# Kernel optimization log

Measured on AMD Instinct MI355X. Metric: run time of the kernel, lower is better.

The kernel has to match this reference:

```python
import jax, jax.numpy as jnp
import numpy as np

B, S, D, H, DH, FF = 2, 2048, 2048, 16, 128, 8192
MAXPOS, EPS, NEG = 2048, 1e-5, -1e9


def _ln(x, g, b):
    m = jnp.mean(x, axis=-1, keepdims=True)
    v = jnp.mean(jnp.square(x - m), axis=-1, keepdims=True)
    return (x - m) * jax.lax.rsqrt(v + EPS) * g + b


def _rope_tables():
    # GPT-J sinusoidal table over rotary_dim = DH
    inv_freq = 1.0 / (10000.0 ** (np.arange(0, DH, 2, dtype=np.float32) / DH))
    ang = np.arange(MAXPOS, dtype=np.float32)[:, None] * inv_freq[None, :]  # [P, DH/2]
    return jnp.asarray(np.sin(ang)), jnp.asarray(np.cos(ang))


def _rotate_every_two(t):
    # t: [B,S,H,DH] -> interleaved (-x1, x0, -x3, x2, ...)
    r = jnp.stack((-t[..., 1::2], t[..., ::2]), axis=-1)
    return r.reshape(t.shape)


def _apply_rope(t, sin, cos):
    # sin/cos: [B,S,DH/2] -> repeat_interleave to [B,S,1,DH]
    sin = jnp.repeat(sin, 2, axis=-1)[:, :, None, :]
    cos = jnp.repeat(cos, 2, axis=-1)[:, :, None, :]
    return t * cos + _rotate_every_two(t) * sin


def setup_inputs() -> dict:
    key = jax.random.key(0)
    ks = jax.random.split(key, 8)
    std = 0.02
    w = lambda k, shape: (jax.random.normal(k, shape, jnp.float32) * std)
    return {
        "hidden_states": jax.random.normal(ks[0], (B, S, D), jnp.float32),
        "position_ids": jnp.tile(jnp.arange(S, dtype=jnp.int32), (B, 1)),
        "wq": w(ks[1], (D, D)),
        "wk": w(ks[2], (D, D)),
        "wv": w(ks[3], (D, D)),
        "wo": w(ks[4], (D, D)),
        "ln1_g": jnp.ones((D,), jnp.float32),
        "ln1_b": jnp.zeros((D,), jnp.float32),
        "ln2_g": jnp.ones((D,), jnp.float32),
        "ln2_b": jnp.zeros((D,), jnp.float32),
        "fc_in_w": w(ks[5], (D, FF)),
        "fc_in_b": jnp.zeros((FF,), jnp.float32),
        "fc_out_w": w(ks[6], (FF, D)),
        "fc_out_b": jnp.zeros((D,), jnp.float32),
    }


def reference(hidden_states, position_ids, wq, wk, wv, wo, ln1_g, ln1_b,
              ln2_g, ln2_b, fc_in_w, fc_in_b, fc_out_w, fc_out_b):
    sin_t, cos_t = _rope_tables()
    h = _ln(hidden_states, ln1_g, ln1_b)
    q = (h @ wq).reshape(B, S, H, DH)
    k = (h @ wk).reshape(B, S, H, DH)
    v = (h @ wv).reshape(B, S, H, DH)
    sin = sin_t[position_ids]  # [B,S,DH/2]
    cos = cos_t[position_ids]
    q = _apply_rope(q, sin, cos)
    k = _apply_rope(k, sin, cos)
    # faithful to source: no 1/sqrt(head_dim) scaling
    scores = jnp.einsum("bqhd,bkhd->bhqk", q, k)
    causal = jnp.tril(jnp.ones((S, S), bool))
    scores = jnp.where(causal[None, None], scores, NEG)
    attn_weights = jax.nn.softmax(scores, axis=-1)
    attn = jnp.einsum("bhqk,bkhd->bqhd", attn_weights, v).reshape(B, S, D)
    attn = attn @ wo
    h2 = _ln(hidden_states + attn, ln2_g, ln2_b)
    ffn = jax.nn.gelu(h2 @ fc_in_w + fc_in_b, approximate=False) @ fc_out_w + fc_out_b
    return h2 + ffn, attn_weights
```

## Files before the change

### kernel.cpp

```cpp
#include <hip/hip_runtime.h>
#include <hip/hip_fp16.h>

#define B_ 2
#define S_ 2048
#define D_ 2048
#define H_ 16
#define DH_ 128
#define FF_ 8192

typedef _Float16 f16x8 __attribute__((ext_vector_type(8)));
typedef float f32x4 __attribute__((ext_vector_type(4)));

#define GLD16(gsrc, ldst) __builtin_amdgcn_global_load_lds( \
    (__attribute__((address_space(1))) void*)(uintptr_t)(gsrc), \
    (__attribute__((address_space(3))) void*)(ldst), 16, 0, 0)

__global__ void build_rope_tab(float* __restrict__ tab) {
  const int pos = blockIdx.x;
  const int i = threadIdx.x;
  float ex = (float)(2 * i) / 128.0f;
  float invf = (float)(1.0 / pow(10000.0, (double)ex));
  float ang = (float)pos * invf;
  tab[(size_t)pos * 128 + 2 * i]     = (float)sin((double)ang);
  tab[(size_t)pos * 128 + 2 * i + 1] = (float)cos((double)ang);
}

__global__ void tcast(const float* __restrict__ in, _Float16* __restrict__ out,
                      int R, int C) {
  __shared__ float tile[32][33];
  const int c0 = blockIdx.x * 32, r0 = blockIdx.y * 32;
  const int tx = threadIdx.x, ty = threadIdx.y;
#pragma unroll
  for (int i = 0; i < 32; i += 8)
    tile[ty + i][tx] = in[(size_t)(r0 + ty + i) * C + c0 + tx];
  __syncthreads();
#pragma unroll
  for (int i = 0; i < 32; i += 8)
    out[(size_t)(c0 + ty + i) * R + r0 + tx] = (_Float16)tile[tx][ty + i];
}

__global__ __launch_bounds__(256) void ln_fused(
    const float* __restrict__ x, const float* __restrict__ add,
    const float* __restrict__ g, const float* __restrict__ bv,
    _Float16* __restrict__ outh, float* __restrict__ outf) {
  const int row = blockIdx.x, tid = threadIdx.x;
  const size_t base = (size_t)row * D_;
  const float4* xp = (const float4*)(x + base) + tid * 2;
  float4 a0 = xp[0], a1 = xp[1];
  if (add) {
    const float4* ap = (const float4*)(add + base) + tid * 2;
    float4 b0 = ap[0], b1 = ap[1];
    a0.x += b0.x; a0.y += b0.y; a0.z += b0.z; a0.w += b0.w;
    a1.x += b1.x; a1.y += b1.y; a1.z += b1.z; a1.w += b1.w;
  }
  float v[8] = {a0.x, a0.y, a0.z, a0.w, a1.x, a1.y, a1.z, a1.w};
  float s1 = 0.f, s2 = 0.f;
#pragma unroll
  for (int j = 0; j < 8; ++j) { s1 += v[j]; s2 += v[j] * v[j]; }
#pragma unroll
  for (int off = 32; off; off >>= 1) {
    s1 += __shfl_xor(s1, off);
    s2 += __shfl_xor(s2, off);
  }
  __shared__ float red[8];
  __shared__ float mv[2];
  if ((tid & 63) == 0) { red[tid >> 6] = s1; red[4 + (tid >> 6)] = s2; }
  __syncthreads();
  if (tid == 0) {
    float t1 = red[0] + red[1] + red[2] + red[3];
    float t2 = red[4] + red[5] + red[6] + red[7];
    float mean = t1 * (1.0f / D_);
    float var = t2 * (1.0f / D_) - mean * mean;
    mv[0] = mean; mv[1] = rsqrtf(var + 1e-5f);
  }
  __syncthreads();
  const float mean = mv[0], rstd = mv[1];
  const int c0 = tid * 8;
#pragma unroll
  for (int j = 0; j < 8; ++j) {
    float nv = (v[j] - mean) * rstd * g[c0 + j] + bv[c0 + j];
    outh[base + c0 + j] = (_Float16)nv;
    if (outf) outf[base + c0 + j] = nv;
  }
}

template <int MODE>
__global__ __launch_bounds__(256) void gemm_bt(
    const _Float16* __restrict__ A, const _Float16* __restrict__ Bt,
    float* __restrict__ outF, _Float16* __restrict__ outH,
    const float* __restrict__ bias, const float* __restrict__ res,
    int M, int N, int K) {
  __shared__ _Float16 lsA[128 * 32];
  __shared__ _Float16 lsB[128 * 32];
  const int tid = threadIdx.x;
  const int w = tid >> 6, l = tid & 63;
  const int l4 = l >> 4, l15 = l & 15;
  const int m0 = blockIdx.y * 128, n0 = blockIdx.x * 128;
  const int wm = (w >> 1) * 64, wn = (w & 1) * 64;
  const int srow = l >> 2, schunk = (l & 3) * 8;
  f32x4 acc[4][4] = {};
  for (int k0 = 0; k0 < K; k0 += 32) {
#pragma unroll
    for (int i = 0; i < 2; ++i) {
      const int ai = w * 2 + i;
      const _Float16* ga = A + (size_t)(m0 + ai * 16 + srow) * K + k0 + schunk;
      GLD16(ga, lsA + ai * 512);
      const _Float16* gb = Bt + (size_t)(n0 + ai * 16 + srow) * K + k0 + schunk;
      GLD16(gb, lsB + ai * 512);
    }
    __syncthreads();
    f16x8 af[4], bf[4];
#pragma unroll
    for (int mi = 0; mi < 4; ++mi)
      af[mi] = *(const f16x8*)(lsA + (wm + mi * 16 + l15) * 32 + l4 * 8);
#pragma unroll
    for (int ni = 0; ni < 4; ++ni)
      bf[ni] = *(const f16x8*)(lsB + (wn + ni * 16 + l15) * 32 + l4 * 8);
#pragma unroll
    for (int mi = 0; mi < 4; ++mi)
#pragma unroll
      for (int ni = 0; ni < 4; ++ni)
        acc[mi][ni] = __builtin_amdgcn_mfma_f32_16x16x32_f16(
            af[mi], bf[ni], acc[mi][ni], 0, 0, 0);
    __syncthreads();
  }
#pragma unroll
  for (int mi = 0; mi < 4; ++mi) {
#pragma unroll
    for (int r = 0; r < 4; ++r) {
      const int row = m0 + wm + mi * 16 + l4 * 4 + r;
#pragma unroll
      for (int ni = 0; ni < 4; ++ni) {
        const int col = n0 + wn + ni * 16 + l15;
        float v = acc[mi][ni][r];
        if (MODE == 0) {
          outH[(size_t)row * N + col] = (_Float16)v;
        } else if (MODE == 1) {
          outF[(size_t)row * N + col] = v;
        } else if (MODE == 2) {
          v += bias[col];
          v = 0.5f * v * (1.0f + erff(v * 0.70710678118654752f));
          outH[(size_t)row * N + col] = (_Float16)v;
        } else {
          v += bias[col] + res[(size_t)row * N + col];
          outF[(size_t)row * N + col] = v;
        }
      }
    }
  }
}

__global__ __launch_bounds__(256) void rope_qk(
    const _Float16* __restrict__ qkv, const int* __restrict__ pos_ids,
    const float* __restrict__ tab, _Float16* __restrict__ qr,
    _Float16* __restrict__ kr) {
  const int tid = threadIdx.x, w = tid >> 6, l = tid & 63;
  const int idx = blockIdx.x * 4 + w;
  const int b = idx >> 11, s = idx & 2047;
  const int pos = pos_ids[idx];
  const int h = l >> 2, qtr = l & 3;
  const float* tp = tab + (size_t)pos * 128 + qtr * 32;
  float sn[16], cs[16];
#pragma unroll
  for (int j = 0; j < 16; ++j) { sn[j] = tp[2 * j]; cs[j] = tp[2 * j + 1]; }
#pragma unroll
  for (int sec = 0; sec < 2; ++sec) {
    const _Float16* src = qkv + (size_t)idx * 6144 + sec * 2048 + h * 128 + qtr * 32;
    int4 dv[4];
    const int4* sp = (const int4*)src;
#pragma unroll
    for (int c = 0; c < 4; ++c) dv[c] = sp[c];
    const _Float16* e = (const _Float16*)dv;
    int4 ov[4];
    _Float16* o = (_Float16*)ov;
#pragma unroll
    for (int j = 0; j < 16; ++j) {
      float x0 = (float)e[2 * j], x1 = (float)e[2 * j + 1];
      o[2 * j]     = (_Float16)(x0 * cs[j] - x1 * sn[j]);
      o[2 * j + 1] = (_Float16)(x1 * cs[j] + x0 * sn[j]);
    }
    _Float16* dst = (sec ? kr : qr) + ((size_t)(b * H_ + h) * S_ + s) * DH_ + qtr * 32;
    int4* dp = (int4*)dst;
#pragma unroll
    for (int c = 0; c < 4; ++c) dp[c] = ov[c];
  }
}

__global__ void vtrans(const _Float16* __restrict__ qkv, _Float16* __restrict__ vt) {
  __shared__ _Float16 tile[32][33];
  const int bh = blockIdx.z;
  const int b = bh >> 4, h = bh & 15;
  const int s0 = blockIdx.x * 32, d0 = blockIdx.y * 32;
  const int tx = threadIdx.x, ty = threadIdx.y;
  const _Float16* src = qkv + (size_t)(b * S_) * 6144 + 4096 + h * 128;
#pragma unroll
  for (int i = 0; i < 32; i += 8)
    tile[ty + i][tx] = src[(size_t)(s0 + ty + i) * 6144 + d0 + tx];
  __syncthreads();
  _Float16* dst = vt + (size_t)bh * DH_ * S_;
#pragma unroll
  for (int i = 0; i < 32; i += 8)
    dst[(size_t)(d0 + ty + i) * S_ + s0 + tx] = tile[tx][ty + i];
}

__global__ __launch_bounds__(256) void attn_flash(
    const _Float16* __restrict__ qr, const _Float16* __restrict__ kr,
    const _Float16* __restrict__ vt, _Float16* __restrict__ attnO,
    float* __restrict__ mOut, float* __restrict__ lOut) {
  __shared__ _Float16 kt_lds[64 * 136];
  __shared__ _Float16 vt_lds[128 * 72];
  __shared__ _Float16 p_lds[4 * 16 * 72];
  const int tid = threadIdx.x, w = tid >> 6, l = tid & 63;
  const int l4 = l >> 4, l15 = l & 15;
  const int qt = blockIdx.x, h = blockIdx.y, b = blockIdx.z;
  const int bh = b * H_ + h;
  const int q0 = qt * 64;
  const int qrowA = q0 + w * 16 + l15;
  f16x8 aq[4];
  const _Float16* qbase = qr + ((size_t)bh * S_ + qrowA) * DH_;
#pragma unroll
  for (int ks = 0; ks < 4; ++ks)
    aq[ks] = *(const f16x8*)(qbase + ks * 32 + l4 * 8);
  float m_r[4], l_r[4];
  f32x4 accO[8] = {};
#pragma unroll
  for (int r = 0; r < 4; ++r) { m_r[r] = -1e30f; l_r[r] = 0.f; }
  const int krow = tid >> 2, kc4 = tid & 3;
  const int vdh = tid >> 1, vc = tid & 1;
  _Float16* pw = p_lds + w * 16 * 72;
  for (int kt = 0; kt <= qt; ++kt) {
    const int kbase = kt * 64;
    {
      const _Float16* src = kr + ((size_t)bh * S_ + kbase + krow) * DH_ + kc4 * 32;
      _Float16* dst = kt_lds + krow * 136 + kc4 * 32;
#pragma unroll
      for (int jj = 0; jj < 4; ++jj)
        *(int4*)(dst + jj * 8) = *(const int4*)(src + jj * 8);
      const _Float16* vsrc = vt + ((size_t)bh * DH_ + vdh) * S_ + kbase + vc * 32;
      _Float16* vdst = vt_lds + vdh * 72 + vc * 32;
#pragma unroll
      for (int jj = 0; jj < 4; ++jj)
        *(int4*)(vdst + jj * 8) = *(const int4*)(vsrc + jj * 8);
    }
    __syncthreads();
    f32x4 sc[4] = {};
#pragma unroll
    for (int ni = 0; ni < 4; ++ni)
#pragma unroll
      for (int ks = 0; ks < 4; ++ks) {
        f16x8 bk = *(const f16x8*)(kt_lds + (ni * 16 + l15) * 136 + ks * 32 + l4 * 8);
        sc[ni] = __builtin_amdgcn_mfma_f32_16x16x32_f16(aq[ks], bk, sc[ni], 0, 0, 0);
      }
    if (kt == qt) {
#pragma unroll
      for (int ni = 0; ni < 4; ++ni)
#pragma unroll
        for (int r = 0; r < 4; ++r) {
          const int col = kbase + ni * 16 + l15;
          const int rowq = q0 + w * 16 + l4 * 4 + r;
          if (col > rowq) sc[ni][r] = -1e30f;
        }
    }
    float scale_r[4];
#pragma unroll
    for (int r = 0; r < 4; ++r) {
      float tmax = fmaxf(fmaxf(sc[0][r], sc[1][r]), fmaxf(sc[2][r], sc[3][r]));
#pragma unroll
      for (int off = 1; off < 16; off <<= 1)
        tmax = fmaxf(tmax, __shfl_xor(tmax, off));
      const float mnew = fmaxf(m_r[r], tmax);
      const float scl = __expf(m_r[r] - mnew);
      float ps = 0.f;
#pragma unroll
      for (int ni = 0; ni < 4; ++ni) {
        float pv = __expf(sc[ni][r] - mnew);
        sc[ni][r] = pv;
        ps += pv;
      }
#pragma unroll
      for (int off = 1; off < 16; off <<= 1) ps += __shfl_xor(ps, off);
      l_r[r] = l_r[r] * scl + ps;
      m_r[r] = mnew;
      scale_r[r] = scl;
    }
#pragma unroll
    for (int oi = 0; oi < 8; ++oi)
#pragma unroll
      for (int r = 0; r < 4; ++r) accO[oi][r] *= scale_r[r];
#pragma unroll
    for (int ni = 0; ni < 4; ++ni)
#pragma unroll
      for (int r = 0; r < 4; ++r)
        pw[(l4 * 4 + r) * 72 + ni * 16 + l15] = (_Float16)sc[ni][r];
#pragma unroll
    for (int ks2 = 0; ks2 < 2; ++ks2) {
      f16x8 pa = *(const f16x8*)(pw + l15 * 72 + ks2 * 32 + l4 * 8);
#pragma unroll
      for (int oi = 0; oi < 8; ++oi) {
        f16x8 bv = *(const f16x8*)(vt_lds + (oi * 16 + l15) * 72 + ks2 * 32 + l4 * 8);
        accO[oi] = __builtin_amdgcn_mfma_f32_16x16x32_f16(pa, bv, accO[oi], 0, 0, 0);
      }
    }
    __syncthreads();
  }
#pragma unroll
  for (int r = 0; r < 4; ++r) {
    const float inv = 1.0f / l_r[r];
    const int rowq = q0 + w * 16 + l4 * 4 + r;
#pragma unroll
    for (int oi = 0; oi < 8; ++oi) {
      attnO[((size_t)(b * S_ + rowq) * H_ + h) * DH_ + oi * 16 + l15] =
          (_Float16)(accO[oi][r] * inv);
    }
    if (l15 == 0) {
      mOut[(size_t)bh * S_ + rowq] = m_r[r];
      lOut[(size_t)bh * S_ + rowq] = l_r[r];
    }
  }
}

__global__ __launch_bounds__(256) void attn_pwrite(
    const _Float16* __restrict__ qr, const _Float16* __restrict__ kr,
    const float* __restrict__ mIn, const float* __restrict__ lIn,
    float* __restrict__ outP) {
  __shared__ _Float16 kt_lds[64 * 136];
  const int tid = threadIdx.x, w = tid >> 6, l = tid & 63;
  const int l4 = l >> 4, l15 = l & 15;
  const int kt = blockIdx.x, qt = blockIdx.y, bh = blockIdx.z;
  const int q0 = qt * 64, kbase = kt * 64;
  float* tileout = outP + ((size_t)bh * S_ + q0) * S_ + kbase;
  if (kt > qt) {
    const int r = tid >> 2, cc = (tid & 3) * 16;
    float4 z = {0.f, 0.f, 0.f, 0.f};
    float4* dst = (float4*)(tileout + (size_t)r * S_ + cc);
#pragma unroll
    for (int i = 0; i < 4; ++i) dst[i] = z;
    return;
  }
  {
    const int krow = tid >> 2, kc4 = tid & 3;
    const _Float16* src = kr + ((size_t)bh * S_ + kbase + krow) * DH_ + kc4 * 32;
    _Float16* dst = kt_lds + krow * 136 + kc4 * 32;
#pragma unroll
    for (int jj = 0; jj < 4; ++jj)
      *(int4*)(dst + jj * 8) = *(const int4*)(src + jj * 8);
  }
  const int qrowA = q0 + w * 16 + l15;
  f16x8 aq[4];
  const _Float16* qbase = qr + ((size_t)bh * S_ + qrowA) * DH_;
#pragma unroll
  for (int ks = 0; ks < 4; ++ks)
    aq[ks] = *(const f16x8*)(qbase + ks * 32 + l4 * 8);
  __syncthreads();
  f32x4 sc[4] = {};
#pragma unroll
  for (int ni = 0; ni < 4; ++ni)
#pragma unroll
    for (int ks = 0; ks < 4; ++ks) {
      f16x8 bk = *(const f16x8*)(kt_lds + (ni * 16 + l15) * 136 + ks * 32 + l4 * 8);
      sc[ni] = __builtin_amdgcn_mfma_f32_16x16x32_f16(aq[ks], bk, sc[ni], 0, 0, 0);
    }
  const bool diag = (kt == qt);
#pragma unroll
  for (int r = 0; r < 4; ++r) {
    const int rowq = q0 + w * 16 + l4 * 4 + r;
    const float mv = mIn[(size_t)bh * S_ + rowq];
    const float linv = 1.0f / lIn[(size_t)bh * S_ + rowq];
#pragma unroll
    for (int ni = 0; ni < 4; ++ni) {
      const int col = kbase + ni * 16 + l15;
      float pv = __expf(sc[ni][r] - mv) * linv;
      if (diag && col > rowq) pv = 0.f;
      tileout[(size_t)(w * 16 + l4 * 4 + r) * S_ + ni * 16 + l15] = pv;
    }
  }
}

extern "C" void kernel_launch(void* const* d_in, const int* in_sizes, int n_in,
                              void* d_out, int out_size, void* d_ws, size_t ws_size,
                              hipStream_t stream) {
  (void)in_sizes; (void)n_in; (void)out_size; (void)ws_size;
  const float* hidden   = (const float*)d_in[0];
  const int*   pos_ids  = (const int*)d_in[1];
  const float* wq       = (const float*)d_in[2];
  const float* wk       = (const float*)d_in[3];
  const float* wv       = (const float*)d_in[4];
  const float* wo       = (const float*)d_in[5];
  const float* ln1_g    = (const float*)d_in[6];
  const float* ln1_b    = (const float*)d_in[7];
  const float* ln2_g    = (const float*)d_in[8];
  const float* ln2_b    = (const float*)d_in[9];
  const float* fc_in_w  = (const float*)d_in[10];
  const float* fc_in_b  = (const float*)d_in[11];
  const float* fc_out_w = (const float*)d_in[12];
  const float* fc_out_b = (const float*)d_in[13];

  float* out1 = (float*)d_out;
  float* outP = out1 + (size_t)B_ * S_ * D_;

  char* ws = (char*)d_ws;
  size_t off = 0;
  auto alloc = [&](size_t bytes) {
    char* p = ws + off;
    off += (bytes + 255) & ~(size_t)255;
    return p;
  };
  _Float16* h1h     = (_Float16*)alloc((size_t)4096 * 2048 * 2);
  _Float16* qkvT    = (_Float16*)alloc((size_t)6144 * 2048 * 2);
  _Float16* woT     = (_Float16*)alloc((size_t)2048 * 2048 * 2);
  _Float16* fc_inT  = (_Float16*)alloc((size_t)8192 * 2048 * 2);
  _Float16* fc_outT = (_Float16*)alloc((size_t)2048 * 8192 * 2);
  _Float16* qkv     = (_Float16*)alloc((size_t)4096 * 6144 * 2);
  _Float16* qrB     = (_Float16*)alloc((size_t)32 * 2048 * 128 * 2);
  _Float16* krB     = (_Float16*)alloc((size_t)32 * 2048 * 128 * 2);
  _Float16* vtB     = (_Float16*)alloc((size_t)32 * 128 * 2048 * 2);
  _Float16* attnO   = (_Float16*)alloc((size_t)4096 * 2048 * 2);
  float* mbuf = (float*)alloc((size_t)32 * 2048 * 4);
  float* lbuf = (float*)alloc((size_t)32 * 2048 * 4);
  float* rtab = (float*)alloc((size_t)2048 * 128 * 4);
  float*     attn_out = (float*)h1h;
  _Float16*  ffn1     = qkv;
  float*     h2f      = (float*)krB;
  _Float16*  h2h      = attnO;

  const dim3 tb(32, 8);
  build_rope_tab<<<2048, 64, 0, stream>>>(rtab);
  tcast<<<dim3(64, 64), tb, 0, stream>>>(wq, qkvT, 2048, 2048);
  tcast<<<dim3(64, 64), tb, 0, stream>>>(wk, qkvT + (size_t)2048 * 2048, 2048, 2048);
  tcast<<<dim3(64, 64), tb, 0, stream>>>(wv, qkvT + (size_t)4096 * 2048, 2048, 2048);
  tcast<<<dim3(64, 64), tb, 0, stream>>>(wo, woT, 2048, 2048);
  tcast<<<dim3(256, 64), tb, 0, stream>>>(fc_in_w, fc_inT, 2048, 8192);
  tcast<<<dim3(64, 256), tb, 0, stream>>>(fc_out_w, fc_outT, 8192, 2048);
  ln_fused<<<4096, 256, 0, stream>>>(hidden, nullptr, ln1_g, ln1_b, h1h, nullptr);
  gemm_bt<0><<<dim3(48, 32), 256, 0, stream>>>(h1h, qkvT, nullptr, qkv,
                                               nullptr, nullptr, 4096, 6144, 2048);
  rope_qk<<<1024, 256, 0, stream>>>(qkv, pos_ids, rtab, qrB, krB);
  vtrans<<<dim3(64, 4, 32), tb, 0, stream>>>(qkv, vtB);
  attn_flash<<<dim3(32, 16, 2), 256, 0, stream>>>(qrB, krB, vtB, attnO, mbuf, lbuf);
  attn_pwrite<<<dim3(32, 32, 32), 256, 0, stream>>>(qrB, krB, mbuf, lbuf, outP);
  gemm_bt<1><<<dim3(16, 32), 256, 0, stream>>>(attnO, woT, attn_out, nullptr,
                                               nullptr, nullptr, 4096, 2048, 2048);
  ln_fused<<<4096, 256, 0, stream>>>(hidden, attn_out, ln2_g, ln2_b, h2h, h2f);
  gemm_bt<2><<<dim3(64, 32), 256, 0, stream>>>(h2h, fc_inT, nullptr, ffn1,
                                               fc_in_b, nullptr, 4096, 8192, 2048);
  gemm_bt<3><<<dim3(16, 32), 256, 0, stream>>>(ffn1, fc_outT, out1, nullptr,
                                               fc_out_b, h2f, 4096, 2048, 8192);
}
```

Baseline: 1.785 ms.

## Swizzle block order, XOR-swizzle LDS, prefetch K/V, lazy softmax rescale in attention

The GEMM and flash-attention kernels remap block IDs so consecutive workgroups spread across tiles, likely to improve L2 or XCD locality. The K/V LDS tiles drop row padding and use an XOR swizzle to avoid bank conflicts. The flash kernel now prefetches the next K/V tile into registers while computing the current one. Online softmax only rescales when the running max grows by more than 8, and skips the accumulator rescale when no lane in the wave needs it. These steps add register pressure and rely on the lazy-max threshold staying numerically safe in fp16 P.

```diff
diff --git a/kernel.cpp b/kernel.cpp
--- a/kernel.cpp
+++ b/kernel.cpp
@@ -95,7 +95,11 @@
   const int tid = threadIdx.x;
   const int w = tid >> 6, l = tid & 63;
   const int l4 = l >> 4, l15 = l & 15;
-  const int m0 = blockIdx.y * 128, n0 = blockIdx.x * 128;
+  const int nbx = gridDim.x;
+  const int nwg = nbx * gridDim.y;
+  const int orig = blockIdx.y * nbx + blockIdx.x;
+  const int swz = (orig & 7) * (nwg >> 3) + (orig >> 3);
+  const int m0 = (swz / nbx) * 128, n0 = (swz % nbx) * 128;
   const int wm = (w >> 1) * 64, wn = (w & 1) * 64;
   const int srow = l >> 2, schunk = (l & 3) * 8;
   f32x4 acc[4][4] = {};
@@ -207,14 +211,17 @@
     const _Float16* __restrict__ qr, const _Float16* __restrict__ kr,
     const _Float16* __restrict__ vt, _Float16* __restrict__ attnO,
     float* __restrict__ mOut, float* __restrict__ lOut) {
-  __shared__ _Float16 kt_lds[64 * 136];
-  __shared__ _Float16 vt_lds[128 * 72];
+  __shared__ _Float16 kt_lds[64 * 128];
+  __shared__ _Float16 vt_lds[128 * 64];
   __shared__ _Float16 p_lds[4 * 16 * 72];
   const int tid = threadIdx.x, w = tid >> 6, l = tid & 63;
   const int l4 = l >> 4, l15 = l & 15;
-  const int qt = blockIdx.x, h = blockIdx.y, b = blockIdx.z;
+  const int orig = (blockIdx.z * 16 + blockIdx.y) * 32 + blockIdx.x;
+  const int swzid = (orig & 7) * 128 + (orig >> 3);
+  const int qt = swzid & 31, h = (swzid >> 5) & 15, b = swzid >> 9;
   const int bh = b * H_ + h;
   const int q0 = qt * 64;
+  const int swzk = (l15 & 7) << 4;
   const int qrowA = q0 + w * 16 + l15;
   f16x8 aq[4];
   const _Float16* qbase = qr + ((size_t)bh * S_ + qrowA) * DH_;
@@ -225,30 +232,42 @@
   f32x4 accO[8] = {};
 #pragma unroll
   for (int r = 0; r < 4; ++r) { m_r[r] = -1e30f; l_r[r] = 0.f; }
-  const int krow = tid >> 2, kc4 = tid & 3;
-  const int vdh = tid >> 1, vc = tid & 1;
+  const int krow_s = tid >> 2, kcol_s = (tid & 3) * 32;
+  const int vrow_s = tid >> 1, vcol_s = (tid & 1) * 32;
   _Float16* pw = p_lds + w * 16 * 72;
+  {
+    const _Float16* ksrc = kr + ((size_t)bh * S_ + krow_s) * DH_ + kcol_s;
+    const _Float16* vsrc = vt + ((size_t)bh * DH_ + vrow_s) * S_ + vcol_s;
+#pragma unroll
+    for (int j = 0; j < 4; ++j) {
+      int4 t0 = *(const int4*)(ksrc + j * 8);
+      int4 t1 = *(const int4*)(vsrc + j * 8);
+      *(int4*)((char*)kt_lds + (krow_s * 256 + ((kcol_s * 2 + j * 16) ^ ((krow_s & 7) << 4)))) = t0;
+      *(int4*)((char*)vt_lds + (vrow_s * 128 + ((vcol_s * 2 + j * 16) ^ ((vrow_s & 7) << 4)))) = t1;
+    }
+  }
+  __syncthreads();
   for (int kt = 0; kt <= qt; ++kt) {
     const int kbase = kt * 64;
-    {
-      const _Float16* src = kr + ((size_t)bh * S_ + kbase + krow) * DH_ + kc4 * 32;
-      _Float16* dst = kt_lds + krow * 136 + kc4 * 32;
-#pragma unroll
-      for (int jj = 0; jj < 4; ++jj)
-        *(int4*)(dst + jj * 8) = *(const int4*)(src + jj * 8);
-      const _Float16* vsrc = vt + ((size_t)bh * DH_ + vdh) * S_ + kbase + vc * 32;
-      _Float16* vdst = vt_lds + vdh * 72 + vc * 32;
-#pragma unroll
-      for (int jj = 0; jj < 4; ++jj)
-        *(int4*)(vdst + jj * 8) = *(const int4*)(vsrc + jj * 8);
-    }
-    __syncthreads();
+    const bool pre = (kt < qt);
+    int4 kreg[4], vreg[4];
+    if (pre) {
+      const int kb2 = kbase + 64;
+      const _Float16* ksrc = kr + ((size_t)bh * S_ + kb2 + krow_s) * DH_ + kcol_s;
+      const _Float16* vsrc = vt + ((size_t)bh * DH_ + vrow_s) * S_ + kb2 + vcol_s;
+#pragma unroll
+      for (int j = 0; j < 4; ++j) {
+        kreg[j] = *(const int4*)(ksrc + j * 8);
+        vreg[j] = *(const int4*)(vsrc + j * 8);
+      }
+    }
     f32x4 sc[4] = {};
 #pragma unroll
     for (int ni = 0; ni < 4; ++ni)
 #pragma unroll
       for (int ks = 0; ks < 4; ++ks) {
-        f16x8 bk = *(const f16x8*)(kt_lds + (ni * 16 + l15) * 136 + ks * 32 + l4 * 8);
+        f16x8 bk = *(const f16x8*)((const char*)kt_lds +
+                     ((ni * 16 + l15) * 256 + ((ks * 64 + l4 * 16) ^ swzk)));
         sc[ni] = __builtin_amdgcn_mfma_f32_16x16x32_f16(aq[ks], bk, sc[ni], 0, 0, 0);
       }
     if (kt == qt) {
@@ -262,31 +281,37 @@
         }
     }
     float scale_r[4];
+    bool need = false;
 #pragma unroll
     for (int r = 0; r < 4; ++r) {
       float tmax = fmaxf(fmaxf(sc[0][r], sc[1][r]), fmaxf(sc[2][r], sc[3][r]));
 #pragma unroll
       for (int off = 1; off < 16; off <<= 1)
         tmax = fmaxf(tmax, __shfl_xor(tmax, off));
-      const float mnew = fmaxf(m_r[r], tmax);
-      const float scl = __expf(m_r[r] - mnew);
+      float scl;
+      if (tmax > m_r[r] + 8.0f) {
+        scl = __expf(m_r[r] - tmax); m_r[r] = tmax; need = true;
+      } else {
+        scl = 1.0f;
+      }
       float ps = 0.f;
 #pragma unroll
       for (int ni = 0; ni < 4; ++ni) {
-        float pv = __expf(sc[ni][r] - mnew);
+        float pv = __expf(sc[ni][r] - m_r[r]);
         sc[ni][r] = pv;
         ps += pv;
       }
 #pragma unroll
       for (int off = 1; off < 16; off <<= 1) ps += __shfl_xor(ps, off);
       l_r[r] = l_r[r] * scl + ps;
-      m_r[r] = mnew;
       scale_r[r] = scl;
     }
-#pragma unroll
-    for (int oi = 0; oi < 8; ++oi)
-#pragma unroll
-      for (int r = 0; r < 4; ++r) accO[oi][r] *= scale_r[r];
+    if (__any((int)need)) {
+#pragma unroll
+      for (int oi = 0; oi < 8; ++oi)
+#pragma unroll
+        for (int r = 0; r < 4; ++r) accO[oi][r] *= scale_r[r];
+    }
 #pragma unroll
     for (int ni = 0; ni < 4; ++ni)
 #pragma unroll
@@ -297,11 +322,20 @@
       f16x8 pa = *(const f16x8*)(pw + l15 * 72 + ks2 * 32 + l4 * 8);
 #pragma unroll
       for (int oi = 0; oi < 8; ++oi) {
-        f16x8 bv = *(const f16x8*)(vt_lds + (oi * 16 + l15) * 72 + ks2 * 32 + l4 * 8);
+        f16x8 bv = *(const f16x8*)((const char*)vt_lds +
+                     ((oi * 16 + l15) * 128 + ((ks2 * 64 + l4 * 16) ^ swzk)));
         accO[oi] = __builtin_amdgcn_mfma_f32_16x16x32_f16(pa, bv, accO[oi], 0, 0, 0);
       }
     }
     __syncthreads();
+    if (pre) {
+#pragma unroll
+      for (int j = 0; j < 4; ++j) {
+        *(int4*)((char*)kt_lds + (krow_s * 256 + ((kcol_s * 2 + j * 16) ^ ((krow_s & 7) << 4)))) = kreg[j];
+        *(int4*)((char*)vt_lds + (vrow_s * 128 + ((vcol_s * 2 + j * 16) ^ ((vrow_s & 7) << 4)))) = vreg[j];
+      }
+      __syncthreads();
+    }
   }
 #pragma unroll
   for (int r = 0; r < 4; ++r) {
@@ -323,11 +357,12 @@
     const _Float16* __restrict__ qr, const _Float16* __restrict__ kr,
     const float* __restrict__ mIn, const float* __restrict__ lIn,
     float* __restrict__ outP) {
-  __shared__ _Float16 kt_lds[64 * 136];
+  __shared__ _Float16 kt_lds[64 * 128];
   const int tid = threadIdx.x, w = tid >> 6, l = tid & 63;
   const int l4 = l >> 4, l15 = l & 15;
   const int kt = blockIdx.x, qt = blockIdx.y, bh = blockIdx.z;
   const int q0 = qt * 64, kbase = kt * 64;
+  const int swzk = (l15 & 7) << 4;
   float* tileout = outP + ((size_t)bh * S_ + q0) * S_ + kbase;
   if (kt > qt) {
     const int r = tid >> 2, cc = (tid & 3) * 16;
@@ -338,12 +373,13 @@
     return;
   }
   {
-    const int krow = tid >> 2, kc4 = tid & 3;
-    const _Float16* src = kr + ((size_t)bh * S_ + kbase + krow) * DH_ + kc4 * 32;
-    _Float16* dst = kt_lds + krow * 136 + kc4 * 32;
-#pragma unroll
-    for (int jj = 0; jj < 4; ++jj)
-      *(int4*)(dst + jj * 8) = *(const int4*)(src + jj * 8);
+    const int krow = tid >> 2, kc = (tid & 3) * 32;
+    const _Float16* src = kr + ((size_t)bh * S_ + kbase + krow) * DH_ + kc;
+#pragma unroll
+    for (int jj = 0; jj < 4; ++jj) {
+      int4 t = *(const int4*)(src + jj * 8);
+      *(int4*)((char*)kt_lds + (krow * 256 + ((kc * 2 + jj * 16) ^ ((krow & 7) << 4)))) = t;
+    }
   }
   const int qrowA = q0 + w * 16 + l15;
   f16x8 aq[4];
@@ -357,7 +393,8 @@
   for (int ni = 0; ni < 4; ++ni)
 #pragma unroll
     for (int ks = 0; ks < 4; ++ks) {
-      f16x8 bk = *(const f16x8*)(kt_lds + (ni * 16 + l15) * 136 + ks * 32 + l4 * 8);
+      f16x8 bk = *(const f16x8*)((const char*)kt_lds +
+                   ((ni * 16 + l15) * 256 + ((ks * 64 + l4 * 16) ^ swzk)));
       sc[ni] = __builtin_amdgcn_mfma_f32_16x16x32_f16(aq[ks], bk, sc[ni], 0, 0, 0);
     }
   const bool diag = (kt == qt);
```

Result: slower. 1.853 ms (+3.8%).
